# Optimization experiments

Measured on AMD Instinct MI355X. Metric: run time of the kernel, lower is better.

## Reference

```python
import jax, jax.numpy as jnp
import numpy as np

N_NODES = 100000
N_EDGES = 1600000
F_IN = 128
F_OUT = 32
HEADS = 8
ALPHA = 0.2  # LeakyReLU slope


def setup_inputs() -> dict:
    key = jax.random.key(0)
    ks = jax.random.split(key, 7)
    x = jax.random.normal(ks[0], (N_NODES, F_IN), dtype=jnp.float32)
    row = jnp.sort(jax.random.randint(ks[1], (N_EDGES,), 0, N_NODES, dtype=jnp.int32))
    col = jax.random.randint(ks[2], (N_EDGES,), 0, N_NODES, dtype=jnp.int32)
    kernels = jax.random.normal(ks[3], (HEADS, F_IN, F_OUT), dtype=jnp.float32) * 0.1
    att_self = jax.random.normal(ks[4], (HEADS, F_OUT), dtype=jnp.float32) * 0.1
    att_neigh = jax.random.normal(ks[5], (HEADS, F_OUT), dtype=jnp.float32) * 0.1
    biases = jax.random.normal(ks[6], (HEADS, F_OUT), dtype=jnp.float32) * 0.1
    return {"x": x, "row": row, "col": col, "kernels": kernels,
            "att_self": att_self, "att_neigh": att_neigh, "biases": biases}


def reference(x, row, col, kernels, att_self, att_neigh, biases):
    # GraphAttention (GAT), eval mode (dropout inactive), concat over heads.
    N = x.shape[0]
    outs = []
    for h in range(kernels.shape[0]):  # fixed small head loop
        feat = x @ kernels[h]                     # [N, F_OUT]
        a_s = feat @ att_self[h]                  # [N]
        a_n = feat @ att_neigh[h]                 # [N]
        e = a_s[row] + a_n[col]                   # [E] edge logits (SDDMM)
        e = jnp.where(e > 0, e, ALPHA * e)        # LeakyReLU(0.2)
        # row-wise (destination-node) sparse softmax, numerically stable
        m = jax.ops.segment_max(e, row, num_segments=N)
        ex = jnp.exp(e - m[row])
        denom = jax.ops.segment_sum(ex, row, num_segments=N)
        alpha = ex / denom[row]                   # [E]
        # SpMM: out[i] = sum_{e: row[e]=i} alpha[e] * feat[col[e]]
        msg = alpha[:, None] * feat[col]          # [E, F_OUT]
        out = jax.ops.segment_sum(msg, row, num_segments=N) + biases[h]
        outs.append(out)
    return jnp.concatenate(outs, axis=1)          # [N, HEADS*F_OUT]
```

## Files before the change

### kernel.cpp

```cpp
#include <hip/hip_runtime.h>
#include <hip/hip_bf16.h>
#include <math.h>


#define F_IN   128
#define F_ALL  256
#define HEADS  8
#define F_OUT  32
#define ALPHA  0.2f

using f32x4  = __attribute__((ext_vector_type(4))) float;
using bf16x8 = __attribute__((ext_vector_type(8))) short;
using u16x8  = __attribute__((ext_vector_type(8))) unsigned short;

static __device__ __forceinline__ unsigned short f32_to_bf16(float f) {
  union { float f; unsigned u; } v; v.f = f;
  unsigned r = v.u + 0x7FFF + ((v.u >> 16) & 1);
  return (unsigned short)(r >> 16);
}
static __device__ __forceinline__ unsigned cvt_pk_bf16(float lo, float hi) {
  unsigned r;
  asm("v_cvt_pk_bf16_f32 %0, %1, %2" : "=v"(r) : "v"(lo), "v"(hi));
  return r;
}
static __device__ __forceinline__ float bf16_lo(unsigned d) {
  return __uint_as_float(d << 16);
}
static __device__ __forceinline__ float bf16_hi(unsigned d) {
  return __uint_as_float(d & 0xffff0000u);
}

__global__ __launch_bounds__(256) void prep(const float* __restrict__ x,
                                            const float* __restrict__ kern,
                                            const float* __restrict__ att_s,
                                            const float* __restrict__ att_n,
                                            const int* __restrict__ row,
                                            unsigned short* __restrict__ xb,
                                            unsigned short* __restrict__ Wt,
                                            float* __restrict__ ws,
                                            float* __restrict__ wn,
                                            int* __restrict__ ptr,
                                            int total_x8, int N, int E) {
  int id = blockIdx.x * 256 + threadIdx.x;
  if (id < total_x8) {
    const float4* x4 = reinterpret_cast<const float4*>(x);
    float4 v0 = x4[(size_t)id * 2], v1 = x4[(size_t)id * 2 + 1];
    u16x8 o;
    o[0] = f32_to_bf16(v0.x); o[1] = f32_to_bf16(v0.y);
    o[2] = f32_to_bf16(v0.z); o[3] = f32_to_bf16(v0.w);
    o[4] = f32_to_bf16(v1.x); o[5] = f32_to_bf16(v1.y);
    o[6] = f32_to_bf16(v1.z); o[7] = f32_to_bf16(v1.w);
    *reinterpret_cast<u16x8*>(xb + (size_t)id * 8) = o;
  }
  if (id < F_ALL * F_IN) {
    int c = id >> 7, k = id & 127;
    Wt[id] = f32_to_bf16(kern[(size_t)(c >> 5) * (F_IN * F_OUT) + k * F_OUT + (c & 31)]);
  }
  if (id < 2 * HEADS * F_IN) {
    int which = id >> 10;
    int hk = id & 1023;
    int h = hk >> 7, k = hk & 127;
    const float* att = which ? att_n : att_s;
    float s = 0.f;
#pragma unroll
    for (int f = 0; f < F_OUT; ++f)
      s += kern[(size_t)h * (F_IN * F_OUT) + k * F_OUT + f] * att[h * F_OUT + f];
    (which ? wn : ws)[hk] = s;
  }
  if (id <= N) {
    int lo = 0, hi = E;
    while (lo < hi) {
      int mid = (lo + hi) >> 1;
      if (row[mid] < id) lo = mid + 1; else hi = mid;
    }
    ptr[id] = lo;
  }
}

__global__ __launch_bounds__(256) void gemm_aproj(
    const unsigned short* __restrict__ xb,
    const unsigned short* __restrict__ Wt,
    const float* __restrict__ x,
    const float* __restrict__ ws, const float* __restrict__ wn,
    unsigned short* __restrict__ featb,
    float* __restrict__ a_s, float* __restrict__ a_n,
    int N, int gemm_blocks, int aproj_waves) {
  const int t = threadIdx.x;

  if ((int)blockIdx.x < gemm_blocks) {
    const int w  = t >> 6;
    const int l  = t & 63;
    const int lr = l & 15;
    const int lq = l >> 4;
    const int n0 = blockIdx.x * 64 + w * 16;

    f32x4 acc[16];
#pragma unroll
    for (int ct = 0; ct < 16; ++ct) acc[ct] = (f32x4){0.f, 0.f, 0.f, 0.f};

    int ar = n0 + lr; if (ar >= N) ar = N - 1;
    const unsigned short* xrow = xb + (size_t)ar * F_IN + lq * 8;
    bf16x8 xfr[4];
#pragma unroll
    for (int kc = 0; kc < 4; ++kc)
      xfr[kc] = *reinterpret_cast<const bf16x8*>(xrow + kc * 32);

#pragma unroll
    for (int ct = 0; ct < 16; ++ct) {
      const unsigned short* wrow = Wt + (size_t)(ct * 16 + lr) * F_IN + lq * 8;
#pragma unroll
      for (int kc = 0; kc < 4; ++kc) {
        bf16x8 wfr = *reinterpret_cast<const bf16x8*>(wrow + kc * 32);
        acc[ct] = __builtin_amdgcn_mfma_f32_16x16x32_bf16(wfr, xfr[kc], acc[ct], 0, 0, 0);
      }
    }
    if (n0 + lr < N) {
      unsigned short* frow = featb + (size_t)ar * F_ALL + lq * 4;
#pragma unroll
      for (int ct = 0; ct < 16; ++ct) {
        uint2 v;
        v.x = cvt_pk_bf16(acc[ct][0], acc[ct][1]);
        v.y = cvt_pk_bf16(acc[ct][2], acc[ct][3]);
        *reinterpret_cast<uint2*>(frow + ct * 16) = v;
      }
    }
    return;
  }

  const int l = t & 63;
  const int o = l & 15, q = l >> 4;
  const int wid = (((int)blockIdx.x - gemm_blocks) * 256 + t) >> 6;

  const float* wrow = (o < 8 ? ws + o * F_IN : wn + (o - 8) * F_IN) + q * 32;
  float4 wv[8];
#pragma unroll
  for (int i = 0; i < 8; i++) wv[i] = reinterpret_cast<const float4*>(wrow)[i];

  for (int n = wid; n < N; n += aproj_waves) {
    const float4* xr = reinterpret_cast<const float4*>(x + (size_t)n * F_IN + q * 32);
    float acc = 0.f;
#pragma unroll
    for (int i = 0; i < 8; i++) {
      float4 xv = xr[i];
      acc += xv.x * wv[i].x + xv.y * wv[i].y + xv.z * wv[i].z + xv.w * wv[i].w;
    }
    acc += __shfl_xor(acc, 16);
    acc += __shfl_xor(acc, 32);
    if (l < 16) {
      if (o < 8) a_s[n * HEADS + o] = acc;
      else       a_n[n * HEADS + (o - 8)] = acc;
    }
  }
}

__global__ __launch_bounds__(256) void gat_scatter(
    const unsigned short* __restrict__ featb,
    const float* __restrict__ a_s, const float* __restrict__ a_n,
    const int* __restrict__ col, const int* __restrict__ ptr,
    const float* __restrict__ biases, float* __restrict__ out, int N) {
  const int t  = threadIdx.x;
  const int n  = blockIdx.x * 4 + (t >> 6);
  if (n >= N) return;
  const int l  = t & 63;
  const int j  = l >> 4;
  const int q  = l & 15;
  const int h0 = 2 * j + (q >> 3);
  const int obase = j * 64 + q * 4;
  const size_t dbase = (size_t)j * 32 + q * 2;

  const int start = ptr[n];
  const int deg   = ptr[n + 1] - start;

  const float4 bv = *reinterpret_cast<const float4*>(&biases[obase]);
  if (deg == 0) {
    *reinterpret_cast<float4*>(&out[(size_t)n * F_ALL + obase]) = bv;
    return;
  }

  const float as = a_s[n * HEADS + h0];
  const unsigned* fu32 = reinterpret_cast<const unsigned*>(featb);

  float a0 = 0.f, a1 = 0.f, a2 = 0.f, a3 = 0.f, sm = 0.f;

  if (deg <= 32) {
    const int le = l & 31;
    int creg = (le < deg) ? col[start + le] : 0;
#pragma unroll 4
    for (int e = 0; e < deg; ++e) {
      int c = __shfl(creg, e, 32);
      float an = a_n[c * HEADS + h0];
      float v = as + an;
      v = v > 0.f ? v : ALPHA * v;
      float w = __expf(v);
      sm += w;
      uint2 d = *reinterpret_cast<const uint2*>(fu32 + (size_t)c * 128 + dbase);
      a0 = fmaf(w, bf16_lo(d.x), a0);
      a1 = fmaf(w, bf16_hi(d.x), a1);
      a2 = fmaf(w, bf16_lo(d.y), a2);
      a3 = fmaf(w, bf16_hi(d.y), a3);
    }
  } else {
    for (int e = 0; e < deg; ++e) {
      int c = col[start + e];
      float an = a_n[c * HEADS + h0];
      float v = as + an;
      v = v > 0.f ? v : ALPHA * v;
      float w = __expf(v);
      sm += w;
      uint2 d = *reinterpret_cast<const uint2*>(fu32 + (size_t)c * 128 + dbase);
      a0 = fmaf(w, bf16_lo(d.x), a0);
      a1 = fmaf(w, bf16_hi(d.x), a1);
      a2 = fmaf(w, bf16_lo(d.y), a2);
      a3 = fmaf(w, bf16_hi(d.y), a3);
    }
  }

  const float inv = 1.0f / sm;
  float4 o = {a0 * inv + bv.x, a1 * inv + bv.y, a2 * inv + bv.z, a3 * inv + bv.w};
  *reinterpret_cast<float4*>(&out[(size_t)n * F_ALL + obase]) = o;
}

extern "C" void kernel_launch(void* const* d_in, const int* in_sizes, int n_in,
                              void* d_out, int out_size, void* d_ws, size_t ws_size,
                              hipStream_t stream) {
  const float* x      = (const float*)d_in[0];
  const int*   row    = (const int*)d_in[1];
  const int*   col    = (const int*)d_in[2];
  const float* kern   = (const float*)d_in[3];
  const float* att_s  = (const float*)d_in[4];
  const float* att_n  = (const float*)d_in[5];
  const float* biases = (const float*)d_in[6];

  const int N = in_sizes[0] / F_IN;
  const int E = in_sizes[1];

  unsigned short* featb = (unsigned short*)d_ws;
  unsigned short* xb    = featb + (size_t)N * F_ALL;
  unsigned short* Wt    = xb + (size_t)N * F_IN;
  float* ws  = (float*)(Wt + F_ALL * F_IN);
  float* wn  = ws + HEADS * F_IN;
  float* a_s = wn + HEADS * F_IN;
  float* a_n = a_s + (size_t)N * HEADS;
  int*   ptr = (int*)(a_n + (size_t)N * HEADS);
  float* out = (float*)d_out;

  const int total_x8     = N * F_IN / 8;
  const int gemm_blocks  = (N + 63) / 64;
  const int aproj_blocks = 1024;
  const int aproj_waves  = aproj_blocks * 4;

  hipLaunchKernelGGL(prep, dim3((total_x8 + 255) / 256), dim3(256), 0, stream,
                     x, kern, att_s, att_n, row, xb, Wt, ws, wn, ptr, total_x8, N, E);
  hipLaunchKernelGGL(gemm_aproj, dim3(gemm_blocks + aproj_blocks), dim3(256), 0, stream,
                     xb, Wt, x, ws, wn, featb, a_s, a_n, N, gemm_blocks, aproj_waves);
  hipLaunchKernelGGL(gat_scatter, dim3((N + 3) / 4), dim3(256), 0, stream,
                     featb, a_s, a_n, col, ptr, biases, out, N);
}
```

Baseline: 260.1 us.

## Split feature matrix into head-pair planes and parallelize edges within waves

The GEMM now writes bf16 features as four planes, one per head pair, each a compact [N,64] array, instead of interleaved [N,256] rows. The scatter kernel launches four times as many blocks, each handling one head-pair plane. Within a wave, the four 16-lane groups process different edges, and partial sums are reduced with cross-lane shuffles. The aim is a smaller working set per plane for better L2 reuse and more memory-level parallelism per wave. The cost is reloading col, ptr and a_s for every plane, plus the extra shuffle reduction.

Result: slower. 329.4 us (+26.7%).

```diff
diff --git a/kernel.cpp b/kernel.cpp
--- a/kernel.cpp
+++ b/kernel.cpp
@@ -115,13 +115,14 @@
       }
     }
     if (n0 + lr < N) {
-      unsigned short* frow = featb + (size_t)ar * F_ALL + lq * 4;
 #pragma unroll
       for (int ct = 0; ct < 16; ++ct) {
+        unsigned short* dst = featb + ((size_t)(ct >> 2) * N + ar) * 64
+                              + (ct & 3) * 16 + lq * 4;
         uint2 v;
         v.x = cvt_pk_bf16(acc[ct][0], acc[ct][1]);
         v.y = cvt_pk_bf16(acc[ct][2], acc[ct][3]);
-        *reinterpret_cast<uint2*>(frow + ct * 16) = v;
+        *reinterpret_cast<uint2*>(dst) = v;
       }
     }
     return;
@@ -158,66 +159,67 @@
     const float* __restrict__ a_s, const float* __restrict__ a_n,
     const int* __restrict__ col, const int* __restrict__ ptr,
     const float* __restrict__ biases, float* __restrict__ out, int N) {
+  const int b  = blockIdx.x;
+  const int p  = (b >> 1) & 3;
+  const int ng = (b >> 3) * 2 + (b & 1);
   const int t  = threadIdx.x;
-  const int n  = blockIdx.x * 4 + (t >> 6);
+  const int n  = ng * 4 + (t >> 6);
   if (n >= N) return;
   const int l  = t & 63;
-  const int j  = l >> 4;
+  const int es = l >> 4;
   const int q  = l & 15;
-  const int h0 = 2 * j + (q >> 3);
-  const int obase = j * 64 + q * 4;
-  const size_t dbase = (size_t)j * 32 + q * 2;
+  const int h  = 2 * p + (q >> 3);
+  const int ob = p * 64 + q * 4;
 
   const int start = ptr[n];
   const int deg   = ptr[n + 1] - start;
 
-  const float4 bv = *reinterpret_cast<const float4*>(&biases[obase]);
   if (deg == 0) {
-    *reinterpret_cast<float4*>(&out[(size_t)n * F_ALL + obase]) = bv;
+    if (l < 16)
+      *reinterpret_cast<float4*>(&out[(size_t)n * F_ALL + ob]) =
+          *reinterpret_cast<const float4*>(&biases[ob]);
     return;
   }
 
-  const float as = a_s[n * HEADS + h0];
-  const unsigned* fu32 = reinterpret_cast<const unsigned*>(featb);
-
-  float a0 = 0.f, a1 = 0.f, a2 = 0.f, a3 = 0.f, sm = 0.f;
-
-  if (deg <= 32) {
+  const float as = a_s[n * HEADS + h];
+  const unsigned* fpl = reinterpret_cast<const unsigned*>(featb) + (size_t)p * N * 32;
+
+  float a0 = 0.f, a1 = 0.f, a2 = 0.f, a3 = 0.f, smp = 0.f;
+
+  for (int cs = 0; cs < deg; cs += 32) {
     const int le = l & 31;
-    int creg = (le < deg) ? col[start + le] : 0;
-#pragma unroll 4
-    for (int e = 0; e < deg; ++e) {
-      int c = __shfl(creg, e, 32);
-      float an = a_n[c * HEADS + h0];
-      float v = as + an;
-      v = v > 0.f ? v : ALPHA * v;
-      float w = __expf(v);
-      sm += w;
-      uint2 d = *reinterpret_cast<const uint2*>(fu32 + (size_t)c * 128 + dbase);
-      a0 = fmaf(w, bf16_lo(d.x), a0);
-      a1 = fmaf(w, bf16_hi(d.x), a1);
-      a2 = fmaf(w, bf16_lo(d.y), a2);
-      a3 = fmaf(w, bf16_hi(d.y), a3);
-    }
-  } else {
-    for (int e = 0; e < deg; ++e) {
-      int c = col[start + e];
-      float an = a_n[c * HEADS + h0];
-      float v = as + an;
-      v = v > 0.f ? v : ALPHA * v;
-      float w = __expf(v);
-      sm += w;
-      uint2 d = *reinterpret_cast<const uint2*>(fu32 + (size_t)c * 128 + dbase);
-      a0 = fmaf(w, bf16_lo(d.x), a0);
-      a1 = fmaf(w, bf16_hi(d.x), a1);
-      a2 = fmaf(w, bf16_lo(d.y), a2);
-      a3 = fmaf(w, bf16_hi(d.y), a3);
-    }
-  }
-
-  const float inv = 1.0f / sm;
-  float4 o = {a0 * inv + bv.x, a1 * inv + bv.y, a2 * inv + bv.z, a3 * inv + bv.w};
-  *reinterpret_cast<float4*>(&out[(size_t)n * F_ALL + obase]) = o;
+    int creg = (cs + le < deg) ? col[start + cs + le] : 0;
+    const int wl = (deg - cs) < 32 ? (deg - cs) : 32;
+#pragma unroll 2
+    for (int e0 = 0; e0 < wl; e0 += 4) {
+      int ei = e0 + es;
+      int c  = __shfl(creg, ei, 32);
+      if (ei < wl) {
+        float v = as + a_n[c * HEADS + h];
+        v = v > 0.f ? v : ALPHA * v;
+        float w = __expf(v);
+        smp += w;
+        uint2 d = *reinterpret_cast<const uint2*>(fpl + (size_t)c * 32 + q * 2);
+        a0 = fmaf(w, bf16_lo(d.x), a0);
+        a1 = fmaf(w, bf16_hi(d.x), a1);
+        a2 = fmaf(w, bf16_lo(d.y), a2);
+        a3 = fmaf(w, bf16_hi(d.y), a3);
+      }
+    }
+  }
+
+  a0 += __shfl_xor(a0, 16); a0 += __shfl_xor(a0, 32);
+  a1 += __shfl_xor(a1, 16); a1 += __shfl_xor(a1, 32);
+  a2 += __shfl_xor(a2, 16); a2 += __shfl_xor(a2, 32);
+  a3 += __shfl_xor(a3, 16); a3 += __shfl_xor(a3, 32);
+  smp += __shfl_xor(smp, 16); smp += __shfl_xor(smp, 32);
+
+  if (l < 16) {
+    const float inv = 1.0f / smp;
+    const float4 bv = *reinterpret_cast<const float4*>(&biases[ob]);
+    float4 o = {a0 * inv + bv.x, a1 * inv + bv.y, a2 * inv + bv.z, a3 * inv + bv.w};
+    *reinterpret_cast<float4*>(&out[(size_t)n * F_ALL + ob]) = o;
+  }
 }
 
 extern "C" void kernel_launch(void* const* d_in, const int* in_sizes, int n_in,
@@ -249,10 +251,14 @@
   const int aproj_blocks = 1024;
   const int aproj_waves  = aproj_blocks * 4;
 
+  const int ngroups   = (N + 3) / 4;
+  const int ngpad     = (ngroups + 1) & ~1;
+  const int scat_blocks = ngpad * 4;
+
   hipLaunchKernelGGL(prep, dim3((total_x8 + 255) / 256), dim3(256), 0, stream,
                      x, kern, att_s, att_n, row, xb, Wt, ws, wn, ptr, total_x8, N, E);
   hipLaunchKernelGGL(gemm_aproj, dim3(gemm_blocks + aproj_blocks), dim3(256), 0, stream,
                      xb, Wt, x, ws, wn, featb, a_s, a_n, N, gemm_blocks, aproj_waves);
-  hipLaunchKernelGGL(gat_scatter, dim3((N + 3) / 4), dim3(256), 0, stream,
+  hipLaunchKernelGGL(gat_scatter, dim3(scat_blocks), dim3(256), 0, stream,
                      featb, a_s, a_n, col, ptr, biases, out, N);
 }
```
